# Kernel tuning notes

Hardware: AMD Instinct MI355X
Metric: run time of the kernel (lower is better)

## Reference

```python
import jax, jax.numpy as jnp
import numpy as np

BN_EPS = 1e-5


def grid_sample_bilinear(img, grid):
    """Torch F.grid_sample, mode=bilinear, padding_mode=zeros, align_corners=False.
    img: (B, C, H, W); grid: (B, N, 2) in [-1, 1] -> (B, C, N)."""
    B, C, H, W = img.shape
    x = ((grid[..., 0] + 1.0) * W - 1.0) * 0.5  # (B, N) pixel coords
    y = ((grid[..., 1] + 1.0) * H - 1.0) * 0.5
    x0 = jnp.floor(x)
    y0 = jnp.floor(y)
    x1 = x0 + 1.0
    y1 = y0 + 1.0
    wx1 = x - x0
    wx0 = 1.0 - wx1
    wy1 = y - y0
    wy0 = 1.0 - wy1
    img_flat = img.reshape(B, C, H * W)

    def corner(xi, yi, w):
        valid = (xi >= 0) & (xi <= W - 1) & (yi >= 0) & (yi <= H - 1)
        xi_c = jnp.clip(xi, 0, W - 1).astype(jnp.int32)
        yi_c = jnp.clip(yi, 0, H - 1).astype(jnp.int32)
        idx = yi_c * W + xi_c  # (B, N)
        vals = jnp.take_along_axis(img_flat, idx[:, None, :], axis=2)  # (B, C, N)
        return vals * (w * valid.astype(img.dtype))[:, None, :]

    return (corner(x0, y0, wx0 * wy0) + corner(x1, y0, wx1 * wy0)
            + corner(x0, y1, wx0 * wy1) + corner(x1, y1, wx1 * wy1))


def conv1x1(x, w, b):
    # x: (B, Cin, N), w: (Cout, Cin), b: (Cout,)
    return jnp.einsum('oi,bin->bon', w, x) + b[None, :, None]


def batchnorm1d_train(x, gamma, beta):
    # training-mode BN over (batch, length) per channel, biased variance
    mean = jnp.mean(x, axis=(0, 2), keepdims=True)
    var = jnp.mean((x - mean) ** 2, axis=(0, 2), keepdims=True)
    xn = (x - mean) * jax.lax.rsqrt(var + BN_EPS)
    return xn * gamma[None, :, None] + beta[None, :, None]


def setup_inputs() -> dict:
    key = jax.random.key(0)
    ks = jax.random.split(key, 12)
    B, N, CI, CP, H, W, R = 4, 16384, 256, 256, 64, 160, 4
    Cin = CI + CP
    Cb = CP // R

    def glorot(k, shape):
        fan_in = shape[1]
        return jax.random.normal(k, shape, dtype=jnp.float32) * (1.0 / np.sqrt(fan_in))

    return {
        'pts_img': jax.random.uniform(ks[0], (B, N, 2), dtype=jnp.float32, minval=-1.0, maxval=1.0),
        'img_feats': jax.random.normal(ks[1], (B, CI, H, W), dtype=jnp.float32),
        'pts_feats': jax.random.normal(ks[2], (B, CP, N), dtype=jnp.float32),
        'fusion_w': glorot(ks[3], (CP, Cin)),
        'fusion_b': jax.random.normal(ks[4], (CP,), dtype=jnp.float32) * 0.01,
        'bn_gamma': jnp.ones((CP,), dtype=jnp.float32),
        'bn_beta': jnp.zeros((CP,), dtype=jnp.float32),
        'ca1_w': glorot(ks[5], (Cb, CP)),
        'ca1_b': jax.random.normal(ks[6], (Cb,), dtype=jnp.float32) * 0.01,
        'ca2_w': glorot(ks[7], (CP, Cb)),
        'ca2_b': jax.random.normal(ks[8], (CP,), dtype=jnp.float32) * 0.01,
        'sa_w': glorot(ks[9], (Cb, CP)),
        'sa_b': jax.random.normal(ks[10], (Cb,), dtype=jnp.float32) * 0.01,
    }


def reference(pts_img, img_feats, pts_feats, fusion_w, fusion_b, bn_gamma, bn_beta,
              ca1_w, ca1_b, ca2_w, ca2_b, sa_w, sa_b):
    # grid_sample gather: (B, C_I, N)
    pts_wise_img_feats = grid_sample_bilinear(img_feats, pts_img)
    fusion = jnp.concatenate([pts_wise_img_feats, pts_feats], axis=1)  # (B, C_I+C_P, N)
    # fusion MLP: conv1x1 + BN + ReLU
    fusion = jax.nn.relu(batchnorm1d_train(conv1x1(fusion, fusion_w, fusion_b), bn_gamma, bn_beta))
    # spatial attention: max over channels of bottleneck conv, sigmoid gate
    spatial = jax.nn.sigmoid(jnp.max(conv1x1(fusion, sa_w, sa_b), axis=1, keepdims=True))
    fusion = spatial * fusion
    # channel attention: bottleneck MLP, global max-pool over points, sigmoid gate
    ca = conv1x1(jax.nn.relu(conv1x1(fusion, ca1_w, ca1_b)), ca2_w, ca2_b)  # (B, C_P, N)
    channel = jax.nn.sigmoid(jnp.max(ca, axis=2, keepdims=True))  # (B, C_P, 1)
    return channel * fusion
```

## Files before the change

### kernel.cpp

```cpp
#include <hip/hip_runtime.h>
#include <stdint.h>


typedef __attribute__((ext_vector_type(8))) short bf16x8;
typedef __attribute__((ext_vector_type(4))) float f32x4;

#define B_ 4
#define N_ 16384
#define H_ 64
#define W_ 160
#define HW_ (H_ * W_)
#define K_ 512

__device__ __forceinline__ float bf2f(unsigned short u) {
    union { unsigned int i; float f; } c; c.i = ((unsigned int)u) << 16; return c.f;
}
__device__ __forceinline__ unsigned short f2bf(float f) {
    union { float f; unsigned int i; } c; c.f = f;
    unsigned int u = c.i;
    return (unsigned short)((u + 0x7FFFu + ((u >> 16) & 1u)) >> 16);
}
__device__ __forceinline__ unsigned int fkey(float f) {
    union { float f; unsigned int u; int i; } c; c.f = f;
    return (c.i < 0) ? ~c.u : (c.u | 0x80000000u);
}
__device__ __forceinline__ float funkey(unsigned int k) {
    union { unsigned int u; float f; } c;
    c.u = (k & 0x80000000u) ? (k & 0x7FFFFFFFu) : ~k;
    return c.f;
}

__device__ __forceinline__ void async_copy16(void* lds, const void* g) {
#if defined(__has_builtin) && __has_builtin(__builtin_amdgcn_global_load_lds)
    __builtin_amdgcn_global_load_lds(
        (const __attribute__((address_space(1))) unsigned int*)g,
        (__attribute__((address_space(3))) unsigned int*)lds, 16, 0, 0);
#else
    *(uint4*)lds = *(const uint4*)g;
#endif
}

__global__ __launch_bounds__(256) void k_imgt(const float* __restrict__ img,
                                              unsigned short* __restrict__ imgT) {
    __shared__ __align__(16) unsigned short tile[64 * 72];
    int t = threadIdx.x;
    int hw0 = blockIdx.x * 64, c0 = blockIdx.y * 64, b = blockIdx.z;
    const float* src = img + ((size_t)b * 256 + c0) * HW_ + hw0;
    int sub = (t & 15) * 4, grp = t >> 4;
#pragma unroll
    for (int it = 0; it < 4; ++it) {
        int cl = grp + it * 16;
        float4 v = *(const float4*)(src + (size_t)cl * HW_ + sub);
        ushort4 o;
        o.x = f2bf(v.x); o.y = f2bf(v.y); o.z = f2bf(v.z); o.w = f2bf(v.w);
        *(ushort4*)(tile + cl * 72 + sub) = o;
    }
    __syncthreads();
    unsigned short* dst = imgT + ((size_t)b * HW_ + hw0) * 256 + c0;
#pragma unroll
    for (int it = 0; it < 4; ++it) {
        int hwl = grp + it * 16;
        ushort4 o;
        o.x = tile[(sub + 0) * 72 + hwl];
        o.y = tile[(sub + 1) * 72 + hwl];
        o.z = tile[(sub + 2) * 72 + hwl];
        o.w = tile[(sub + 3) * 72 + hwl];
        *(ushort4*)(dst + (size_t)hwl * 256 + sub) = o;
    }
}

__global__ __launch_bounds__(256) void k_xt(const float* __restrict__ pim,
                                            const unsigned short* __restrict__ imgT,
                                            const float* __restrict__ pts,
                                            unsigned short* __restrict__ XT,
                                            const float* __restrict__ fw,
                                            const float* __restrict__ saw,
                                            const float* __restrict__ c1w,
                                            const float* __restrict__ c2w,
                                            unsigned short* WfB, unsigned short* saB,
                                            unsigned short* ca1B, unsigned short* ca2B,
                                            float* buckets, unsigned int* camax) {
    __shared__ __align__(16) unsigned short tile[64 * 72];
    int t = threadIdx.x;
    int bx = blockIdx.x;
    if (bx < 4096) {
        int w = t >> 6, lane = t & 63;
        int p0 = bx * 16 + w * 4;
        int c = lane * 4;
        for (int pp = 0; pp < 4; ++pp) {
            int p = p0 + pp;
            int b = p >> 14;
            float gx = pim[(size_t)p * 2 + 0];
            float gy = pim[(size_t)p * 2 + 1];
            float x = (gx + 1.0f) * (0.5f * W_) - 0.5f;
            float y = (gy + 1.0f) * (0.5f * H_) - 0.5f;
            float xf = floorf(x), yf = floorf(y);
            float wx1 = x - xf, wx0 = 1.0f - wx1;
            float wy1 = y - yf, wy0 = 1.0f - wy1;
            int x0 = (int)xf, y0 = (int)yf;
            int x1 = x0 + 1, y1 = y0 + 1;
            float vx0 = (x0 >= 0 && x0 < W_) ? 1.f : 0.f;
            float vx1 = (x1 >= 0 && x1 < W_) ? 1.f : 0.f;
            float vy0 = (y0 >= 0 && y0 < H_) ? 1.f : 0.f;
            float vy1 = (y1 >= 0 && y1 < H_) ? 1.f : 0.f;
            int cx0 = min(max(x0, 0), W_ - 1), cx1 = min(max(x1, 0), W_ - 1);
            int cy0 = min(max(y0, 0), H_ - 1), cy1 = min(max(y1, 0), H_ - 1);
            float w00 = wx0 * wy0 * vx0 * vy0;
            float w10 = wx1 * wy0 * vx1 * vy0;
            float w01 = wx0 * wy1 * vx0 * vy1;
            float w11 = wx1 * wy1 * vx1 * vy1;
            const unsigned short* base = imgT + (size_t)b * HW_ * 256;
            ushort4 a00 = *(const ushort4*)(base + ((size_t)cy0 * W_ + cx0) * 256 + c);
            ushort4 a10 = *(const ushort4*)(base + ((size_t)cy0 * W_ + cx1) * 256 + c);
            ushort4 a01 = *(const ushort4*)(base + ((size_t)cy1 * W_ + cx0) * 256 + c);
            ushort4 a11 = *(const ushort4*)(base + ((size_t)cy1 * W_ + cx1) * 256 + c);
            ushort4 o;
            o.x = f2bf(w00 * bf2f(a00.x) + w10 * bf2f(a10.x) + w01 * bf2f(a01.x) + w11 * bf2f(a11.x));
            o.y = f2bf(w00 * bf2f(a00.y) + w10 * bf2f(a10.y) + w01 * bf2f(a01.y) + w11 * bf2f(a11.y));
            o.z = f2bf(w00 * bf2f(a00.z) + w10 * bf2f(a10.z) + w01 * bf2f(a01.z) + w11 * bf2f(a11.z));
            o.w = f2bf(w00 * bf2f(a00.w) + w10 * bf2f(a10.w) + w01 * bf2f(a01.w) + w11 * bf2f(a11.w));
            *(ushort4*)(XT + (size_t)p * K_ + c) = o;
        }
    } else if (bx < 8192) {
        int j = bx - 4096;
        int n0 = (j & 255) * 64, c0 = ((j >> 8) & 3) * 64, b = j >> 10;
        const float* src = pts + ((size_t)b * 256 + c0) * N_ + n0;
        int sub = (t & 15) * 4, grp = t >> 4;
#pragma unroll
        for (int it = 0; it < 4; ++it) {
            int cl = grp + it * 16;
            float4 v = *(const float4*)(src + (size_t)cl * N_ + sub);
            ushort4 o;
            o.x = f2bf(v.x); o.y = f2bf(v.y); o.z = f2bf(v.z); o.w = f2bf(v.w);
            *(ushort4*)(tile + cl * 72 + sub) = o;
        }
        __syncthreads();
        unsigned short* dst = XT + ((size_t)b * N_ + n0) * K_ + 256 + c0;
#pragma unroll
        for (int it = 0; it < 4; ++it) {
            int nl = grp + it * 16;
            ushort4 o;
            o.x = tile[(sub + 0) * 72 + nl];
            o.y = tile[(sub + 1) * 72 + nl];
            o.z = tile[(sub + 2) * 72 + nl];
            o.w = tile[(sub + 3) * 72 + nl];
            *(ushort4*)(dst + (size_t)nl * K_ + sub) = o;
        }
    } else {
        int j = bx - 8192;
        if (j == 0) {
            for (int i = t; i < 16 * 512; i += 256) buckets[i] = 0.f;
            for (int i = t; i < 8 * 1024; i += 256) camax[i] = 0u;
        }
        int i = j * 256 + t;
        if (i < 131072) WfB[i] = f2bf(fw[i]);
        else if (i < 147456) saB[i - 131072] = f2bf(saw[i - 131072]);
        else if (i < 163840) ca1B[i - 147456] = f2bf(c1w[i - 147456]);
        else if (i < 180224) ca2B[i - 163840] = f2bf(c2w[i - 163840]);
    }
}

__global__ __launch_bounds__(256, 2) void k_gemm1(const unsigned short* __restrict__ WfB,
                                                  const unsigned short* __restrict__ XT,
                                                  const float* __restrict__ fb,
                                                  unsigned short* __restrict__ Y,
                                                  float* __restrict__ buckets) {
    __shared__ __align__(16) unsigned short At[128 * 32];
    __shared__ __align__(16) unsigned short Bt[128 * 32];
    __shared__ float biasS[128];
    __shared__ float redS[2][128], redQ[2][128];
    int t = threadIdx.x;
    int n0 = blockIdx.x * 128, m0 = blockIdx.y * 128, b = blockIdx.z;
    if (t < 128) biasS[t] = fb[m0 + t];
    const unsigned short* Xb = XT + (size_t)b * N_ * K_;
    int w = t >> 6, lane = t & 63, quad = lane >> 4, l15 = lane & 15;
    int wm = w >> 1, wn = w & 1;
    int srow = lane >> 2, scol = (lane & 3) * 8;
    const f32x4 fzero = {0.f, 0.f, 0.f, 0.f};
    f32x4 acc[4][4];
#pragma unroll
    for (int i = 0; i < 4; ++i)
#pragma unroll
        for (int j = 0; j < 4; ++j) acc[i][j] = fzero;
    for (int kt = 0; kt < 16; ++kt) {
        int k0 = kt * 32;
        __syncthreads();
#pragma unroll
        for (int cch = 0; cch < 2; ++cch) {
            int chunk = w * 2 + cch;
            int row = chunk * 16 + srow;
            async_copy16(At + chunk * 512 + lane * 8,
                         WfB + (size_t)(m0 + row) * K_ + k0 + scol);
            async_copy16(Bt + chunk * 512 + lane * 8,
                         Xb + (size_t)(n0 + row) * K_ + k0 + scol);
        }
        __syncthreads();
        bf16x8 af[4], bv[4];
#pragma unroll
        for (int i = 0; i < 4; ++i) {
            af[i] = *(const bf16x8*)(At + (wm * 64 + i * 16 + l15) * 32 + quad * 8);
            bv[i] = *(const bf16x8*)(Bt + (wn * 64 + i * 16 + l15) * 32 + quad * 8);
        }
#pragma unroll
        for (int i = 0; i < 4; ++i)
#pragma unroll
            for (int j = 0; j < 4; ++j)
                acc[i][j] = __builtin_amdgcn_mfma_f32_16x16x32_bf16(af[i], bv[j], acc[i][j], 0, 0, 0);
    }
    size_t Yb = (size_t)b * N_ * 256;
#pragma unroll
    for (int i = 0; i < 4; ++i) {
        int mloc = wm * 64 + i * 16 + quad * 4;
        float b0 = biasS[mloc + 0], b1 = biasS[mloc + 1];
        float b2 = biasS[mloc + 2], b3 = biasS[mloc + 3];
        float bb[4] = {b0, b1, b2, b3};
#pragma unroll
        for (int j = 0; j < 4; ++j) {
            int n = n0 + wn * 64 + j * 16 + l15;
            ushort4 o;
            o.x = f2bf(acc[i][j][0] + b0);
            o.y = f2bf(acc[i][j][1] + b1);
            o.z = f2bf(acc[i][j][2] + b2);
            o.w = f2bf(acc[i][j][3] + b3);
            *(ushort4*)(Y + Yb + (size_t)n * 256 + m0 + mloc) = o;
        }
#pragma unroll
        for (int r = 0; r < 4; ++r) {
            float s = 0.f, q = 0.f;
#pragma unroll
            for (int j = 0; j < 4; ++j) {
                float y = acc[i][j][r] + bb[r];
                s += y;
                q += y * y;
            }
#pragma unroll
            for (int d = 1; d < 16; d <<= 1) {
                s += __shfl_xor(s, d, 64);
                q += __shfl_xor(q, d, 64);
            }
            if (l15 == 0) {
                redS[wn][mloc + r] = s;
                redQ[wn][mloc + r] = q;
            }
        }
    }
    __syncthreads();
    if (t < 128) {
        float* bk = buckets + (size_t)(blockIdx.x & 15) * 512;
        atomicAdd(bk + m0 + t, redS[0][t] + redS[1][t]);
        atomicAdd(bk + 256 + m0 + t, redQ[0][t] + redQ[1][t]);
    }
}

__global__ __launch_bounds__(256, 3) void k_gate(unsigned short* __restrict__ F,
                                                 const float* __restrict__ buckets,
                                                 const float* __restrict__ gamma,
                                                 const float* __restrict__ beta,
                                                 const unsigned short* __restrict__ saB,
                                                 const float* __restrict__ sab,
                                                 const unsigned short* __restrict__ c1B,
                                                 const float* __restrict__ c1b,
                                                 const unsigned short* __restrict__ c2B,
                                                 unsigned int* __restrict__ camax) {
    __shared__ __align__(16) unsigned short Ft[64 * 264];
    __shared__ __align__(16) unsigned short Ht[64 * 72];
    __shared__ float scS[256], shS[256];
    __shared__ float sp[64];
    int t = threadIdx.x;
    size_t pts0 = (size_t)blockIdx.x * 64;
    int b = (int)(pts0 >> 14);
    int w = t >> 6, lane = t & 63, quad = lane >> 4, l15 = lane & 15;

    {
        float s = 0.f, q = 0.f;
#pragma unroll
        for (int bk = 0; bk < 16; ++bk) {
            s += buckets[bk * 512 + t];
            q += buckets[bk * 512 + 256 + t];
        }
        const float inv = 1.0f / (float)(B_ * N_);
        float mean = s * inv;
        float var = q * inv - mean * mean;
        float sc = gamma[t] * rsqrtf(var + 1e-5f);
        scS[t] = sc;
        shS[t] = beta[t] - mean * sc;
    }
    __syncthreads();

    int cc = (t * 8) & 255;
    float scr[8], shr[8];
#pragma unroll
    for (int e = 0; e < 8; ++e) { scr[e] = scS[cc + e]; shr[e] = shS[cc + e]; }
    for (int idx = t * 8; idx < 64 * 256; idx += 2048) {
        int r = idx >> 8;
        uint4 v = *(const uint4*)(F + (pts0 + r) * 256 + cc);
        unsigned short* us = (unsigned short*)&v;
#pragma unroll
        for (int e = 0; e < 8; ++e) {
            float f = bf2f(us[e]) * scr[e] + shr[e];
            us[e] = f2bf(fmaxf(f, 0.f));
        }
        *(uint4*)(Ft + r * 264 + cc) = v;
    }
    __syncthreads();

    {
        const f32x4 fzero = {0.f, 0.f, 0.f, 0.f};
        f32x4 acc[4] = {fzero, fzero, fzero, fzero};
        for (int kt = 0; kt < 8; ++kt) {
            int k0 = kt * 32;
            bf16x8 af = *(const bf16x8*)(Ft + (w * 16 + l15) * 264 + k0 + quad * 8);
#pragma unroll
            for (int jt = 0; jt < 4; ++jt) {
                bf16x8 bv = *(const bf16x8*)(saB + (size_t)(jt * 16 + l15) * 256 + k0 + quad * 8);
                acc[jt] = __builtin_amdgcn_mfma_f32_16x16x32_bf16(af, bv, acc[jt], 0, 0, 0);
            }
        }
        float sb[4];
#pragma unroll
        for (int jt = 0; jt < 4; ++jt) sb[jt] = sab[jt * 16 + l15];
#pragma unroll
        for (int r = 0; r < 4; ++r) {
            float v = acc[0][r] + sb[0];
            v = fmaxf(v, acc[1][r] + sb[1]);
            v = fmaxf(v, acc[2][r] + sb[2]);
            v = fmaxf(v, acc[3][r] + sb[3]);
#pragma unroll
            for (int d = 1; d < 16; d <<= 1) v = fmaxf(v, __shfl_xor(v, d, 64));
            if (l15 == 0) sp[w * 16 + quad * 4 + r] = 1.0f / (1.0f + __expf(-v));
        }
    }
    __syncthreads();

    for (int idx = t * 8; idx < 64 * 256; idx += 2048) {
        int r = idx >> 8;
        float s = sp[r];
        uint4 v = *(uint4*)(Ft + r * 264 + cc);
        unsigned short* us = (unsigned short*)&v;
#pragma unroll
        for (int e = 0; e < 8; ++e) us[e] = f2bf(bf2f(us[e]) * s);
        *(uint4*)(Ft + r * 264 + cc) = v;
        *(uint4*)(F + (pts0 + r) * 256 + cc) = v;
    }
    __syncthreads();

    {
        const f32x4 fzero = {0.f, 0.f, 0.f, 0.f};
        f32x4 acc[4] = {fzero, fzero, fzero, fzero};
        for (int kt = 0; kt < 8; ++kt) {
            int k0 = kt * 32;
            bf16x8 af = *(const bf16x8*)(Ft + (w * 16 + l15) * 264 + k0 + quad * 8);
#pragma unroll
            for (int jt = 0; jt < 4; ++jt) {
                bf16x8 bv = *(const bf16x8*)(c1B + (size_t)(jt * 16 + l15) * 256 + k0 + quad * 8);
                acc[jt] = __builtin_amdgcn_mfma_f32_16x16x32_bf16(af, bv, acc[jt], 0, 0, 0);
            }
        }
#pragma unroll
        for (int jt = 0; jt < 4; ++jt) {
            float bb = c1b[jt * 16 + l15];
#pragma unroll
            for (int r = 0; r < 4; ++r) {
                int pt = w * 16 + quad * 4 + r;
                Ht[pt * 72 + jt * 16 + l15] = f2bf(fmaxf(acc[jt][r] + bb, 0.f));
            }
        }
    }
    __syncthreads();

    {
        const f32x4 fzero = {0.f, 0.f, 0.f, 0.f};
        f32x4 acc[4][4];
#pragma unroll
        for (int i = 0; i < 4; ++i)
#pragma unroll
            for (int mt = 0; mt < 4; ++mt) acc[i][mt] = fzero;
#pragma unroll
        for (int kk = 0; kk < 2; ++kk) {
            bf16x8 af[4], bv[4];
#pragma unroll
            for (int i = 0; i < 4; ++i)
                af[i] = *(const bf16x8*)(Ht + (i * 16 + l15) * 72 + kk * 32 + quad * 8);
#pragma unroll
            for (int mt = 0; mt < 4; ++mt)
                bv[mt] = *(const bf16x8*)(c2B + (size_t)(w * 64 + mt * 16 + l15) * 64 + kk * 32 + quad * 8);
#pragma unroll
            for (int i = 0; i < 4; ++i)
#pragma unroll
                for (int mt = 0; mt < 4; ++mt)
                    acc[i][mt] = __builtin_amdgcn_mfma_f32_16x16x32_bf16(af[i], bv[mt], acc[i][mt], 0, 0, 0);
        }
        unsigned int* cam = camax + (size_t)(blockIdx.x & 7) * 1024 + b * 256;
#pragma unroll
        for (int mt = 0; mt < 4; ++mt) {
            float v = acc[0][mt][0];
#pragma unroll
            for (int i = 0; i < 4; ++i)
#pragma unroll
                for (int r = 0; r < 4; ++r) v = fmaxf(v, acc[i][mt][r]);
            v = fmaxf(v, __shfl_xor(v, 16, 64));
            v = fmaxf(v, __shfl_xor(v, 32, 64));
            if (quad == 0) atomicMax(cam + w * 64 + mt * 16 + l15, fkey(v));
        }
    }
}

__global__ __launch_bounds__(256) void k_out(const unsigned short* __restrict__ F,
                                             const unsigned int* __restrict__ camax,
                                             const float* __restrict__ c2b,
                                             float* __restrict__ out) {
    __shared__ __align__(16) unsigned short tile[64 * 72];
    __shared__ float ch[64];
    int t = threadIdx.x;
    int n0 = blockIdx.x * 64, m0 = blockIdx.y * 64, b = blockIdx.z;
    if (t < 64) {
        int m = m0 + t;
        unsigned int k = 0u;
#pragma unroll
        for (int bk = 0; bk < 8; ++bk) k = max(k, camax[bk * 1024 + b * 256 + m]);
        float v = funkey(k) + c2b[m];
        ch[t] = 1.0f / (1.0f + __expf(-v));
    }
    int sub = (t & 15) * 4, grp = t >> 4;
    const unsigned short* src = F + (size_t)b * N_ * 256;
#pragma unroll
    for (int it = 0; it < 4; ++it) {
        int nl = grp + it * 16;
        ushort4 v = *(const ushort4*)(src + (size_t)(n0 + nl) * 256 + m0 + sub);
        *(ushort4*)(tile + nl * 72 + sub) = v;
    }
    __syncthreads();
    float* dst = out + ((size_t)b * 256 + m0) * N_ + n0;
#pragma unroll
    for (int it = 0; it < 4; ++it) {
        int ml = grp + it * 16;
        float g = ch[ml];
        float4 o;
        o.x = bf2f(tile[(sub + 0) * 72 + ml]) * g;
        o.y = bf2f(tile[(sub + 1) * 72 + ml]) * g;
        o.z = bf2f(tile[(sub + 2) * 72 + ml]) * g;
        o.w = bf2f(tile[(sub + 3) * 72 + ml]) * g;
        *(float4*)(dst + (size_t)ml * N_ + sub) = o;
    }
}

extern "C" void kernel_launch(void* const* d_in, const int* in_sizes, int n_in,
                              void* d_out, int out_size, void* d_ws, size_t ws_size,
                              hipStream_t stream) {
    (void)in_sizes; (void)n_in; (void)out_size; (void)ws_size;
    const float* pts_img = (const float*)d_in[0];
    const float* img     = (const float*)d_in[1];
    const float* pts     = (const float*)d_in[2];
    const float* fw      = (const float*)d_in[3];
    const float* fbias   = (const float*)d_in[4];
    const float* gamma   = (const float*)d_in[5];
    const float* beta    = (const float*)d_in[6];
    const float* c1w     = (const float*)d_in[7];
    const float* c1b     = (const float*)d_in[8];
    const float* c2w     = (const float*)d_in[9];
    const float* c2b     = (const float*)d_in[10];
    const float* saw     = (const float*)d_in[11];
    const float* sab     = (const float*)d_in[12];
    float* out = (float*)d_out;

    char* ws = (char*)d_ws;
    unsigned short* XT   = (unsigned short*)(ws);
    unsigned short* imgT = (unsigned short*)(ws + 67108864);
    unsigned short* Y    = (unsigned short*)(ws + 67108864);
    unsigned short* WfB  = (unsigned short*)(ws + 100663296);
    unsigned short* saB  = (unsigned short*)(ws + 100925440);
    unsigned short* ca1B = (unsigned short*)(ws + 100958208);
    unsigned short* ca2B = (unsigned short*)(ws + 100990976);
    float* buckets       = (float*)(ws + 101023744);
    unsigned int* camax  = (unsigned int*)(ws + 101056512);

    k_imgt<<<dim3(160, 4, 4), 256, 0, stream>>>(img, imgT);
    k_xt<<<8896, 256, 0, stream>>>(pts_img, imgT, pts, XT, fw, saw, c1w, c2w,
                                   WfB, saB, ca1B, ca2B, buckets, camax);
    k_gemm1<<<dim3(128, 2, 4), 256, 0, stream>>>(WfB, XT, fbias, Y, buckets);
    k_gate<<<1024, 256, 0, stream>>>(Y, buckets, gamma, beta, saB, sab, ca1B, c1b, ca2B, camax);
    k_out<<<dim3(256, 4, 4), 256, 0, stream>>>(Y, camax, c2b, out);
}
```

Measured before the change: 291.8 us.

## Restructure gate kernel to skip F write-back, recompute BN/gate in output pass

The gate kernel no longer writes the spatially gated activations back to global memory. It stores per-point spatial gates and BN scale/shift instead, and k_out recomputes BN+ReLU+spatial+channel gating from Y. The spatial and ca1 GEMMs are merged into one MFMA pass, using linearity to apply the spatial scale after the ca1 product, with weights preloaded into registers. Separately, the diff reorders gemm1 grid dimensions, batches the gather loads in k_xt with a block-to-batch swizzle, changes the LDS tile padding, and lowers k_gate occupancy to 2. These trade a global write pass for extra registers and recomputation in the output kernel.

```diff
diff --git a/kernel.cpp b/kernel.cpp
--- a/kernel.cpp
+++ b/kernel.cpp
@@ -42,7 +42,7 @@
 
 __global__ __launch_bounds__(256) void k_imgt(const float* __restrict__ img,
                                               unsigned short* __restrict__ imgT) {
-    __shared__ __align__(16) unsigned short tile[64 * 72];
+    __shared__ __align__(16) unsigned short tile[64 * 68];
     int t = threadIdx.x;
     int hw0 = blockIdx.x * 64, c0 = blockIdx.y * 64, b = blockIdx.z;
     const float* src = img + ((size_t)b * 256 + c0) * HW_ + hw0;
@@ -53,7 +53,7 @@
         float4 v = *(const float4*)(src + (size_t)cl * HW_ + sub);
         ushort4 o;
         o.x = f2bf(v.x); o.y = f2bf(v.y); o.z = f2bf(v.z); o.w = f2bf(v.w);
-        *(ushort4*)(tile + cl * 72 + sub) = o;
+        *(ushort4*)(tile + cl * 68 + sub) = o;
     }
     __syncthreads();
     unsigned short* dst = imgT + ((size_t)b * HW_ + hw0) * 256 + c0;
@@ -61,10 +61,10 @@
     for (int it = 0; it < 4; ++it) {
         int hwl = grp + it * 16;
         ushort4 o;
-        o.x = tile[(sub + 0) * 72 + hwl];
-        o.y = tile[(sub + 1) * 72 + hwl];
-        o.z = tile[(sub + 2) * 72 + hwl];
-        o.w = tile[(sub + 3) * 72 + hwl];
+        o.x = tile[(sub + 0) * 68 + hwl];
+        o.y = tile[(sub + 1) * 68 + hwl];
+        o.z = tile[(sub + 2) * 68 + hwl];
+        o.w = tile[(sub + 3) * 68 + hwl];
         *(ushort4*)(dst + (size_t)hwl * 256 + sub) = o;
     }
 }
@@ -80,20 +80,25 @@
                                             unsigned short* WfB, unsigned short* saB,
                                             unsigned short* ca1B, unsigned short* ca2B,
                                             float* buckets, unsigned int* camax) {
-    __shared__ __align__(16) unsigned short tile[64 * 72];
+    __shared__ __align__(16) unsigned short tile[64 * 68];
     int t = threadIdx.x;
     int bx = blockIdx.x;
     if (bx < 4096) {
+        int batch = (bx & 7) >> 1;
+        int loc = (bx >> 3) * 2 + (bx & 1);
         int w = t >> 6, lane = t & 63;
-        int p0 = bx * 16 + w * 4;
+        int p0 = batch * N_ + loc * 16 + w * 4;
         int c = lane * 4;
+        const unsigned short* base = imgT + (size_t)batch * HW_ * 256;
+        float2 g01[4];
+#pragma unroll
+        for (int pp = 0; pp < 4; ++pp) g01[pp] = *(const float2*)(pim + (size_t)(p0 + pp) * 2);
+        ushort4 a00[4], a10[4], a01[4], a11[4];
+        float w00[4], w10[4], w01[4], w11[4];
+#pragma unroll
         for (int pp = 0; pp < 4; ++pp) {
-            int p = p0 + pp;
-            int b = p >> 14;
-            float gx = pim[(size_t)p * 2 + 0];
-            float gy = pim[(size_t)p * 2 + 1];
-            float x = (gx + 1.0f) * (0.5f * W_) - 0.5f;
-            float y = (gy + 1.0f) * (0.5f * H_) - 0.5f;
+            float x = (g01[pp].x + 1.0f) * (0.5f * W_) - 0.5f;
+            float y = (g01[pp].y + 1.0f) * (0.5f * H_) - 0.5f;
             float xf = floorf(x), yf = floorf(y);
             float wx1 = x - xf, wx0 = 1.0f - wx1;
             float wy1 = y - yf, wy0 = 1.0f - wy1;
@@ -105,21 +110,27 @@
             float vy1 = (y1 >= 0 && y1 < H_) ? 1.f : 0.f;
             int cx0 = min(max(x0, 0), W_ - 1), cx1 = min(max(x1, 0), W_ - 1);
             int cy0 = min(max(y0, 0), H_ - 1), cy1 = min(max(y1, 0), H_ - 1);
-            float w00 = wx0 * wy0 * vx0 * vy0;
-            float w10 = wx1 * wy0 * vx1 * vy0;
-            float w01 = wx0 * wy1 * vx0 * vy1;
-            float w11 = wx1 * wy1 * vx1 * vy1;
-            const unsigned short* base = imgT + (size_t)b * HW_ * 256;
-            ushort4 a00 = *(const ushort4*)(base + ((size_t)cy0 * W_ + cx0) * 256 + c);
-            ushort4 a10 = *(const ushort4*)(base + ((size_t)cy0 * W_ + cx1) * 256 + c);
-            ushort4 a01 = *(const ushort4*)(base + ((size_t)cy1 * W_ + cx0) * 256 + c);
-            ushort4 a11 = *(const ushort4*)(base + ((size_t)cy1 * W_ + cx1) * 256 + c);
+            w00[pp] = wx0 * wy0 * vx0 * vy0;
+            w10[pp] = wx1 * wy0 * vx1 * vy0;
+            w01[pp] = wx0 * wy1 * vx0 * vy1;
+            w11[pp] = wx1 * wy1 * vx1 * vy1;
+            a00[pp] = *(const ushort4*)(base + ((size_t)cy0 * W_ + cx0) * 256 + c);
+            a10[pp] = *(const ushort4*)(base + ((size_t)cy0 * W_ + cx1) * 256 + c);
+            a01[pp] = *(const ushort4*)(base + ((size_t)cy1 * W_ + cx0) * 256 + c);
+            a11[pp] = *(const ushort4*)(base + ((size_t)cy1 * W_ + cx1) * 256 + c);
+        }
+#pragma unroll
+        for (int pp = 0; pp < 4; ++pp) {
             ushort4 o;
-            o.x = f2bf(w00 * bf2f(a00.x) + w10 * bf2f(a10.x) + w01 * bf2f(a01.x) + w11 * bf2f(a11.x));
-            o.y = f2bf(w00 * bf2f(a00.y) + w10 * bf2f(a10.y) + w01 * bf2f(a01.y) + w11 * bf2f(a11.y));
-            o.z = f2bf(w00 * bf2f(a00.z) + w10 * bf2f(a10.z) + w01 * bf2f(a01.z) + w11 * bf2f(a11.z));
-            o.w = f2bf(w00 * bf2f(a00.w) + w10 * bf2f(a10.w) + w01 * bf2f(a01.w) + w11 * bf2f(a11.w));
-            *(ushort4*)(XT + (size_t)p * K_ + c) = o;
+            o.x = f2bf(w00[pp] * bf2f(a00[pp].x) + w10[pp] * bf2f(a10[pp].x) +
+                       w01[pp] * bf2f(a01[pp].x) + w11[pp] * bf2f(a11[pp].x));
+            o.y = f2bf(w00[pp] * bf2f(a00[pp].y) + w10[pp] * bf2f(a10[pp].y) +
+                       w01[pp] * bf2f(a01[pp].y) + w11[pp] * bf2f(a11[pp].y));
+            o.z = f2bf(w00[pp] * bf2f(a00[pp].z) + w10[pp] * bf2f(a10[pp].z) +
+                       w01[pp] * bf2f(a01[pp].z) + w11[pp] * bf2f(a11[pp].z));
+            o.w = f2bf(w00[pp] * bf2f(a00[pp].w) + w10[pp] * bf2f(a10[pp].w) +
+                       w01[pp] * bf2f(a01[pp].w) + w11[pp] * bf2f(a11[pp].w));
+            *(ushort4*)(XT + (size_t)(p0 + pp) * K_ + c) = o;
         }
     } else if (bx < 8192) {
         int j = bx - 4096;
@@ -132,7 +143,7 @@
             float4 v = *(const float4*)(src + (size_t)cl * N_ + sub);
             ushort4 o;
             o.x = f2bf(v.x); o.y = f2bf(v.y); o.z = f2bf(v.z); o.w = f2bf(v.w);
-            *(ushort4*)(tile + cl * 72 + sub) = o;
+            *(ushort4*)(tile + cl * 68 + sub) = o;
         }
         __syncthreads();
         unsigned short* dst = XT + ((size_t)b * N_ + n0) * K_ + 256 + c0;
@@ -140,10 +151,10 @@
         for (int it = 0; it < 4; ++it) {
             int nl = grp + it * 16;
             ushort4 o;
-            o.x = tile[(sub + 0) * 72 + nl];
-            o.y = tile[(sub + 1) * 72 + nl];
-            o.z = tile[(sub + 2) * 72 + nl];
-            o.w = tile[(sub + 3) * 72 + nl];
+            o.x = tile[(sub + 0) * 68 + nl];
+            o.y = tile[(sub + 1) * 68 + nl];
+            o.z = tile[(sub + 2) * 68 + nl];
+            o.w = tile[(sub + 3) * 68 + nl];
             *(ushort4*)(dst + (size_t)nl * K_ + sub) = o;
         }
     } else {
@@ -170,7 +181,7 @@
     __shared__ float biasS[128];
     __shared__ float redS[2][128], redQ[2][128];
     int t = threadIdx.x;
-    int n0 = blockIdx.x * 128, m0 = blockIdx.y * 128, b = blockIdx.z;
+    int m0 = blockIdx.x * 128, n0 = blockIdx.y * 128, b = blockIdx.z;
     if (t < 128) biasS[t] = fb[m0 + t];
     const unsigned short* Xb = XT + (size_t)b * N_ * K_;
     int w = t >> 6, lane = t & 63, quad = lane >> 4, l15 = lane & 15;
@@ -246,13 +257,13 @@
     }
     __syncthreads();
     if (t < 128) {
-        float* bk = buckets + (size_t)(blockIdx.x & 15) * 512;
+        float* bk = buckets + (size_t)(blockIdx.y & 15) * 512;
         atomicAdd(bk + m0 + t, redS[0][t] + redS[1][t]);
         atomicAdd(bk + 256 + m0 + t, redQ[0][t] + redQ[1][t]);
     }
 }
 
-__global__ __launch_bounds__(256, 3) void k_gate(unsigned short* __restrict__ F,
+__global__ __launch_bounds__(256, 2) void k_gate(const unsigned short* __restrict__ Y,
                                                  const float* __restrict__ buckets,
                                                  const float* __restrict__ gamma,
                                                  const float* __restrict__ beta,
@@ -261,15 +272,28 @@
                                                  const unsigned short* __restrict__ c1B,
                                                  const float* __restrict__ c1b,
                                                  const unsigned short* __restrict__ c2B,
-                                                 unsigned int* __restrict__ camax) {
+                                                 unsigned int* __restrict__ camax,
+                                                 float* __restrict__ sp_g,
+                                                 float* __restrict__ ss_out) {
     __shared__ __align__(16) unsigned short Ft[64 * 264];
     __shared__ __align__(16) unsigned short Ht[64 * 72];
     __shared__ float scS[256], shS[256];
-    __shared__ float sp[64];
+    __shared__ float saPart[4][64];
+    __shared__ float spL[64];
     int t = threadIdx.x;
     size_t pts0 = (size_t)blockIdx.x * 64;
     int b = (int)(pts0 >> 14);
     int w = t >> 6, lane = t & 63, quad = lane >> 4, l15 = lane & 15;
+    int jrow = w * 16 + l15;
+
+    bf16x8 bvs[8], bvc[8];
+#pragma unroll
+    for (int kt = 0; kt < 8; ++kt) {
+        bvs[kt] = *(const bf16x8*)(saB + (size_t)jrow * 256 + kt * 32 + quad * 8);
+        bvc[kt] = *(const bf16x8*)(c1B + (size_t)jrow * 256 + kt * 32 + quad * 8);
+    }
+    float sbias = sab[jrow];
+    float cbias = c1b[jrow];
 
     {
         float s = 0.f, q = 0.f;
@@ -282,8 +306,10 @@
         float mean = s * inv;
         float var = q * inv - mean * mean;
         float sc = gamma[t] * rsqrtf(var + 1e-5f);
+        float sh = beta[t] - mean * sc;
         scS[t] = sc;
-        shS[t] = beta[t] - mean * sc;
+        shS[t] = sh;
+        if (blockIdx.x == 0) { ss_out[t] = sc; ss_out[256 + t] = sh; }
     }
     __syncthreads();
 
@@ -293,7 +319,7 @@
     for (int e = 0; e < 8; ++e) { scr[e] = scS[cc + e]; shr[e] = shS[cc + e]; }
     for (int idx = t * 8; idx < 64 * 256; idx += 2048) {
         int r = idx >> 8;
-        uint4 v = *(const uint4*)(F + (pts0 + r) * 256 + cc);
+        uint4 v = *(const uint4*)(Y + (pts0 + r) * 256 + cc);
         unsigned short* us = (unsigned short*)&v;
 #pragma unroll
         for (int e = 0; e < 8; ++e) {
@@ -304,100 +330,77 @@
     }
     __syncthreads();
 
+    const f32x4 fzero = {0.f, 0.f, 0.f, 0.f};
+    f32x4 accS[4], accC[4];
+#pragma unroll
+    for (int i = 0; i < 4; ++i) { accS[i] = fzero; accC[i] = fzero; }
+#pragma unroll
+    for (int kt = 0; kt < 8; ++kt) {
+        bf16x8 af[4];
+#pragma unroll
+        for (int i = 0; i < 4; ++i)
+            af[i] = *(const bf16x8*)(Ft + (i * 16 + l15) * 264 + kt * 32 + quad * 8);
+#pragma unroll
+        for (int i = 0; i < 4; ++i) {
+            accS[i] = __builtin_amdgcn_mfma_f32_16x16x32_bf16(af[i], bvs[kt], accS[i], 0, 0, 0);
+            accC[i] = __builtin_amdgcn_mfma_f32_16x16x32_bf16(af[i], bvc[kt], accC[i], 0, 0, 0);
+        }
+    }
+#pragma unroll
+    for (int i = 0; i < 4; ++i) {
+#pragma unroll
+        for (int r = 0; r < 4; ++r) {
+            float v = accS[i][r] + sbias;
+#pragma unroll
+            for (int d = 1; d < 16; d <<= 1) v = fmaxf(v, __shfl_xor(v, d, 64));
+            if (l15 == 0) saPart[w][i * 16 + quad * 4 + r] = v;
+        }
+    }
+    __syncthreads();
+    if (t < 64) {
+        float m4 = fmaxf(fmaxf(saPart[0][t], saPart[1][t]),
+                         fmaxf(saPart[2][t], saPart[3][t]));
+        float sv = 1.0f / (1.0f + __expf(-m4));
+        spL[t] = sv;
+        sp_g[pts0 + t] = sv;
+    }
+    __syncthreads();
+
+#pragma unroll
+    for (int i = 0; i < 4; ++i) {
+#pragma unroll
+        for (int r = 0; r < 4; ++r) {
+            int pt = i * 16 + quad * 4 + r;
+            float hv = fmaxf(accC[i][r] * spL[pt] + cbias, 0.f);
+            Ht[pt * 72 + jrow] = f2bf(hv);
+        }
+    }
+    __syncthreads();
+
     {
-        const f32x4 fzero = {0.f, 0.f, 0.f, 0.f};
-        f32x4 acc[4] = {fzero, fzero, fzero, fzero};
-        for (int kt = 0; kt < 8; ++kt) {
-            int k0 = kt * 32;
-            bf16x8 af = *(const bf16x8*)(Ft + (w * 16 + l15) * 264 + k0 + quad * 8);
-#pragma unroll
-            for (int jt = 0; jt < 4; ++jt) {
-                bf16x8 bv = *(const bf16x8*)(saB + (size_t)(jt * 16 + l15) * 256 + k0 + quad * 8);
-                acc[jt] = __builtin_amdgcn_mfma_f32_16x16x32_bf16(af, bv, acc[jt], 0, 0, 0);
+        bf16x8 b2a[4], b2b[4];
+#pragma unroll
+        for (int mt = 0; mt < 4; ++mt) {
+            b2a[mt] = *(const bf16x8*)(c2B + (size_t)(w * 64 + mt * 16 + l15) * 64 + quad * 8);
+            b2b[mt] = *(const bf16x8*)(c2B + (size_t)(w * 64 + mt * 16 + l15) * 64 + 32 + quad * 8);
+        }
+        float vmax[4] = {-3e38f, -3e38f, -3e38f, -3e38f};
+#pragma unroll
+        for (int i = 0; i < 4; ++i) {
+            bf16x8 a0 = *(const bf16x8*)(Ht + (i * 16 + l15) * 72 + quad * 8);
+            bf16x8 a1 = *(const bf16x8*)(Ht + (i * 16 + l15) * 72 + 32 + quad * 8);
+#pragma unroll
+            for (int mt = 0; mt < 4; ++mt) {
+                f32x4 acc = __builtin_amdgcn_mfma_f32_16x16x32_bf16(a0, b2a[mt], fzero, 0, 0, 0);
+                acc = __builtin_amdgcn_mfma_f32_16x16x32_bf16(a1, b2b[mt], acc, 0, 0, 0);
+#pragma unroll
+                for (int r = 0; r < 4; ++r) vmax[mt] = fmaxf(vmax[mt], acc[r]);
             }
         }
-        float sb[4];
-#pragma unroll
-        for (int jt = 0; jt < 4; ++jt) sb[jt] = sab[jt * 16 + l15];
-#pragma unroll
-        for (int r = 0; r < 4; ++r) {
-            float v = acc[0][r] + sb[0];
-            v = fmaxf(v, acc[1][r] + sb[1]);
-            v = fmaxf(v, acc[2][r] + sb[2]);
-            v = fmaxf(v, acc[3][r] + sb[3]);
-#pragma unroll
-            for (int d = 1; d < 16; d <<= 1) v = fmaxf(v, __shfl_xor(v, d, 64));
-            if (l15 == 0) sp[w * 16 + quad * 4 + r] = 1.0f / (1.0f + __expf(-v));
-        }
-    }
-    __syncthreads();
-
-    for (int idx = t * 8; idx < 64 * 256; idx += 2048) {
-        int r = idx >> 8;
-        float s = sp[r];
-        uint4 v = *(uint4*)(Ft + r * 264 + cc);
-        unsigned short* us = (unsigned short*)&v;
-#pragma unroll
-        for (int e = 0; e < 8; ++e) us[e] = f2bf(bf2f(us[e]) * s);
-        *(uint4*)(Ft + r * 264 + cc) = v;
-        *(uint4*)(F + (pts0 + r) * 256 + cc) = v;
-    }
-    __syncthreads();
-
-    {
-        const f32x4 fzero = {0.f, 0.f, 0.f, 0.f};
-        f32x4 acc[4] = {fzero, fzero, fzero, fzero};
-        for (int kt = 0; kt < 8; ++kt) {
-            int k0 = kt * 32;
-            bf16x8 af = *(const bf16x8*)(Ft + (w * 16 + l15) * 264 + k0 + quad * 8);
-#pragma unroll
-            for (int jt = 0; jt < 4; ++jt) {
-                bf16x8 bv = *(const bf16x8*)(c1B + (size_t)(jt * 16 + l15) * 256 + k0 + quad * 8);
-                acc[jt] = __builtin_amdgcn_mfma_f32_16x16x32_bf16(af, bv, acc[jt], 0, 0, 0);
-            }
-        }
-#pragma unroll
-        for (int jt = 0; jt < 4; ++jt) {
-            float bb = c1b[jt * 16 + l15];
-#pragma unroll
-            for (int r = 0; r < 4; ++r) {
-                int pt = w * 16 + quad * 4 + r;
-                Ht[pt * 72 + jt * 16 + l15] = f2bf(fmaxf(acc[jt][r] + bb, 0.f));
-            }
-        }
-    }
-    __syncthreads();
-
-    {
-        const f32x4 fzero = {0.f, 0.f, 0.f, 0.f};
-        f32x4 acc[4][4];
-#pragma unroll
-        for (int i = 0; i < 4; ++i)
-#pragma unroll
-            for (int mt = 0; mt < 4; ++mt) acc[i][mt] = fzero;
-#pragma unroll
-        for (int kk = 0; kk < 2; ++kk) {
-            bf16x8 af[4], bv[4];
-#pragma unroll
-            for (int i = 0; i < 4; ++i)
-                af[i] = *(const bf16x8*)(Ht + (i * 16 + l15) * 72 + kk * 32 + quad * 8);
-#pragma unroll
-            for (int mt = 0; mt < 4; ++mt)
-                bv[mt] = *(const bf16x8*)(c2B + (size_t)(w * 64 + mt * 16 + l15) * 64 + kk * 32 + quad * 8);
-#pragma unroll
-            for (int i = 0; i < 4; ++i)
-#pragma unroll
-                for (int mt = 0; mt < 4; ++mt)
-                    acc[i][mt] = __builtin_amdgcn_mfma_f32_16x16x32_bf16(af[i], bv[mt], acc[i][mt], 0, 0, 0);
-        }
         unsigned int* cam = camax + (size_t)(blockIdx.x & 7) * 1024 + b * 256;
 #pragma unroll
         for (int mt = 0; mt < 4; ++mt) {
-            float v = acc[0][mt][0];
-#pragma unroll
-            for (int i = 0; i < 4; ++i)
-#pragma unroll
-                for (int r = 0; r < 4; ++r) v = fmaxf(v, acc[i][mt][r]);
+            float v = vmax[mt];
             v = fmaxf(v, __shfl_xor(v, 16, 64));
             v = fmaxf(v, __shfl_xor(v, 32, 64));
             if (quad == 0) atomicMax(cam + w * 64 + mt * 16 + l15, fkey(v));
@@ -405,12 +408,14 @@
     }
 }
 
-__global__ __launch_bounds__(256) void k_out(const unsigned short* __restrict__ F,
+__global__ __launch_bounds__(256) void k_out(const unsigned short* __restrict__ Y,
                                              const unsigned int* __restrict__ camax,
                                              const float* __restrict__ c2b,
+                                             const float* __restrict__ ss,
+                                             const float* __restrict__ sp_g,
                                              float* __restrict__ out) {
-    __shared__ __align__(16) unsigned short tile[64 * 72];
-    __shared__ float ch[64];
+    __shared__ __align__(16) unsigned short tile[64 * 68];
+    __shared__ float ch[64], scT[64], shT[64], spT[64];
     int t = threadIdx.x;
     int n0 = blockIdx.x * 64, m0 = blockIdx.y * 64, b = blockIdx.z;
     if (t < 64) {
@@ -418,28 +423,30 @@
         unsigned int k = 0u;
 #pragma unroll
         for (int bk = 0; bk < 8; ++bk) k = max(k, camax[bk * 1024 + b * 256 + m]);
-        float v = funkey(k) + c2b[m];
-        ch[t] = 1.0f / (1.0f + __expf(-v));
+        ch[t] = 1.0f / (1.0f + __expf(-(funkey(k) + c2b[m])));
+        scT[t] = ss[m];
+        shT[t] = ss[256 + m];
+        spT[t] = sp_g[(size_t)b * N_ + n0 + t];
     }
     int sub = (t & 15) * 4, grp = t >> 4;
-    const unsigned short* src = F + (size_t)b * N_ * 256;
+    const unsigned short* src = Y + ((size_t)b * N_ + n0) * 256 + m0;
 #pragma unroll
     for (int it = 0; it < 4; ++it) {
         int nl = grp + it * 16;
-        ushort4 v = *(const ushort4*)(src + (size_t)(n0 + nl) * 256 + m0 + sub);
-        *(ushort4*)(tile + nl * 72 + sub) = v;
+        ushort4 v = *(const ushort4*)(src + (size_t)nl * 256 + sub);
+        *(ushort4*)(tile + nl * 68 + sub) = v;
     }
     __syncthreads();
     float* dst = out + ((size_t)b * 256 + m0) * N_ + n0;
 #pragma unroll
     for (int it = 0; it < 4; ++it) {
         int ml = grp + it * 16;
-        float g = ch[ml];
+        float g = ch[ml], scv = scT[ml], shv = shT[ml];
         float4 o;
-        o.x = bf2f(tile[(sub + 0) * 72 + ml]) * g;
-        o.y = bf2f(tile[(sub + 1) * 72 + ml]) * g;
-        o.z = bf2f(tile[(sub + 2) * 72 + ml]) * g;
-        o.w = bf2f(tile[(sub + 3) * 72 + ml]) * g;
+        o.x = fmaxf(bf2f(tile[(sub + 0) * 68 + ml]) * scv + shv, 0.f) * spT[sub + 0] * g;
+        o.y = fmaxf(bf2f(tile[(sub + 1) * 68 + ml]) * scv + shv, 0.f) * spT[sub + 1] * g;
+        o.z = fmaxf(bf2f(tile[(sub + 2) * 68 + ml]) * scv + shv, 0.f) * spT[sub + 2] * g;
+        o.w = fmaxf(bf2f(tile[(sub + 3) * 68 + ml]) * scv + shv, 0.f) * spT[sub + 3] * g;
         *(float4*)(dst + (size_t)ml * N_ + sub) = o;
     }
 }
@@ -473,11 +480,14 @@
     unsigned short* ca2B = (unsigned short*)(ws + 100990976);
     float* buckets       = (float*)(ws + 101023744);
     unsigned int* camax  = (unsigned int*)(ws + 101056512);
+    float* sp_g          = (float*)(ws + 101089280);
+    float* ss            = (float*)(ws + 101351424);
 
     k_imgt<<<dim3(160, 4, 4), 256, 0, stream>>>(img, imgT);
     k_xt<<<8896, 256, 0, stream>>>(pts_img, imgT, pts, XT, fw, saw, c1w, c2w,
                                    WfB, saB, ca1B, ca2B, buckets, camax);
-    k_gemm1<<<dim3(128, 2, 4), 256, 0, stream>>>(WfB, XT, fbias, Y, buckets);
-    k_gate<<<1024, 256, 0, stream>>>(Y, buckets, gamma, beta, saB, sab, ca1B, c1b, ca2B, camax);
-    k_out<<<dim3(256, 4, 4), 256, 0, stream>>>(Y, camax, c2b, out);
-}
+    k_gemm1<<<dim3(2, 128, 4), 256, 0, stream>>>(WfB, XT, fbias, Y, buckets);
+    k_gate<<<1024, 256, 0, stream>>>(Y, buckets, gamma, beta, saB, sab, ca1B, c1b,
+                                     ca2B, camax, sp_g, ss);
+    k_out<<<dim3(256, 4, 4), 256, 0, stream>>>(Y, camax, c2b, ss, sp_g, out);
+}
```

After: 270.7 us. 1.08x faster.
